# Performance work log

Hardware: AMD Instinct MI355X
Metric: run time of the kernel (lower is better)

The kernel has to match this reference:

```python
import jax, jax.numpy as jnp
import numpy as np

N_NODES = 100000
N_EDGES = 1600000
N_GRAPHS = 512
DIM = 64


def gcn_conv(x, W, b, src, dst, n):
    # PyG GCNConv: h = x @ W; add self-loops; symmetric norm D^-1/2 (A+I) D^-1/2; aggregate; + bias
    h = x @ W  # [N, H]
    loop = jnp.arange(n, dtype=src.dtype)
    s = jnp.concatenate([src, loop])
    d = jnp.concatenate([dst, loop])
    deg = jax.ops.segment_sum(jnp.ones_like(d, dtype=h.dtype), d, num_segments=n)  # in-degree incl self-loop
    dinv = jnp.where(deg > 0, jax.lax.rsqrt(deg), 0.0)
    norm = dinv[s] * dinv[d]  # [E+N]
    msg = h[s] * norm[:, None]  # gather + scale
    out = jax.ops.segment_sum(msg, d, num_segments=n)  # scatter-add
    return out + b


def global_mean_pool(x, batch, num_graphs):
    sums = jax.ops.segment_sum(x, batch, num_segments=num_graphs)
    cnts = jax.ops.segment_sum(jnp.ones((x.shape[0],), x.dtype), batch, num_segments=num_graphs)
    return sums / jnp.maximum(cnts, 1.0)[:, None]


def setup_inputs() -> dict:
    key = jax.random.key(0)
    ks = jax.random.split(key, 12)
    scale = 1.0 / np.sqrt(DIM)
    x = jax.random.normal(ks[0], (N_NODES, DIM), jnp.float32)
    edge_index = jax.random.randint(ks[1], (2, N_EDGES), 0, N_NODES, dtype=jnp.int64)
    batch = jnp.sort(jax.random.randint(ks[2], (N_NODES,), 0, N_GRAPHS, dtype=jnp.int64))
    W1 = jax.random.normal(ks[3], (DIM, DIM), jnp.float32) * scale
    b1 = jnp.zeros((DIM,), jnp.float32)
    W2 = jax.random.normal(ks[4], (DIM, DIM), jnp.float32) * scale
    b2 = jnp.zeros((DIM,), jnp.float32)
    W3 = jax.random.normal(ks[5], (DIM, DIM), jnp.float32) * scale
    b3 = jnp.zeros((DIM,), jnp.float32)
    W4 = jax.random.normal(ks[6], (DIM, 1), jnp.float32) * scale
    b4 = jnp.zeros((1,), jnp.float32)
    return {"x": x, "edge_index": edge_index, "batch": batch,
            "W1": W1, "b1": b1, "W2": W2, "b2": b2,
            "W3": W3, "b3": b3, "W4": W4, "b4": b4}


def reference(x, edge_index, batch, W1, b1, W2, b2, W3, b3, W4, b4):
    src, dst = edge_index[0], edge_index[1]
    h = gcn_conv(x, W1, b1, src, dst, N_NODES)
    h = jax.nn.relu(h)
    h = gcn_conv(h, W2, b2, src, dst, N_NODES)
    g = global_mean_pool(h, batch, N_GRAPHS)  # [G, H]
    g = jax.nn.relu(g @ W3 + b3)
    pred = (g @ W4 + b4).reshape(-1)  # [G]
    return pred
```

## Files before the change

kernel.cpp:

```cpp
#include <hip/hip_runtime.h>
#include <hip/hip_fp16.h>
#include <math.h>


#define NBLK 3125
#define BCAP 40960

__global__ __launch_bounds__(256) void k_init(float* gsum, int* blockCnt,
                                              int* bucketCursor, int gsz,
                                              int nblk) {
  int i = blockIdx.x * 256 + threadIdx.x;
  if (i < gsz) gsum[i] = 0.f;
  if (i < nblk + 64) blockCnt[i] = 0;
  if (i < 64) bucketCursor[i] = i * BCAP;
}

__global__ __launch_bounds__(256) void k_scan(const int* __restrict__ blockCnt,
                                              int* __restrict__ blockBase,
                                              int* __restrict__ blockCursor,
                                              int nblk) {
  __shared__ int wsum[4];
  int t = threadIdx.x;
  int w = t >> 6, lane = t & 63;
  int ch = (nblk + 255) >> 8;
  int lo = t * ch;
  int hi = lo + ch;
  if (hi > nblk) hi = nblk;
  int s = 0;
  for (int i = lo; i < hi; ++i) s += blockCnt[i];
  int inc = s;
  for (int off = 1; off < 64; off <<= 1) {
    int u = __shfl_up(inc, off);
    if (lane >= off) inc += u;
  }
  if (lane == 63) wsum[w] = inc;
  __syncthreads();
  int wpre = 0;
  for (int i = 0; i < w; ++i) wpre += wsum[i];
  int run = wpre + inc - s;
  for (int i = lo; i < hi; ++i) {
    int v = blockCnt[i];
    blockBase[i] = run;
    blockCursor[i] = run;
    run += v;
  }
  if (t == 0) blockBase[nblk] = wsum[0] + wsum[1] + wsum[2] + wsum[3];
}

__global__ __launch_bounds__(256) void k_p1(const int* __restrict__ src,
                                            const int* __restrict__ dst,
                                            int* __restrict__ bucketCursor,
                                            int* __restrict__ blockCnt,
                                            int* __restrict__ tmp, int e,
                                            int nblk) {
  __shared__ int hist[64];
  __shared__ int gbase[64];
  __shared__ int hB[3200];
  int t = threadIdx.x;
  for (int i = t; i < 3200; i += 256) hB[i] = 0;
  int base0 = blockIdx.x * 4096;
  for (int ph = 0; ph < 2; ++ph) {
    int base = base0 + ph * 2048;
    if (t < 64) hist[t] = 0;
    __syncthreads();
    int ent[8], rk[8], bk[8];
#pragma unroll
    for (int k = 0; k < 8; ++k) {
      int i = base + k * 256 + t;
      bool v = i < e;
      int s = v ? src[i] : 0;
      int d = v ? dst[i] : 0;
      bk[k] = d >> 11;
      ent[k] = (((d >> 5) & 63) << 22) | (s << 5) | (d & 31);
      rk[k] = v ? atomicAdd(&hist[bk[k]], 1) : -1;
      if (v) atomicAdd(&hB[d >> 5], 1);
    }
    __syncthreads();
    if (t < 64 && hist[t] > 0) gbase[t] = atomicAdd(&bucketCursor[t], hist[t]);
    __syncthreads();
#pragma unroll
    for (int k = 0; k < 8; ++k)
      if (rk[k] >= 0) {
        int pos = gbase[bk[k]] + rk[k];
        if (pos < (bk[k] + 1) * BCAP) tmp[pos] = ent[k];
      }
  }
  __syncthreads();
  for (int i = t; i < nblk; i += 256) {
    int v = hB[i];
    if (v) atomicAdd(&blockCnt[i], v);
  }
}

__global__ __launch_bounds__(256) void k_p2(const int* __restrict__ bucketCursor,
                                            const int* __restrict__ tmp,
                                            int* __restrict__ blockCursor,
                                            int* __restrict__ csr, int nblk) {
  __shared__ int hist[64];
  __shared__ int gbase[64];
  int b = blockIdx.x >> 3;
  int sl = blockIdx.x & 7;
  int lo_b = b * BCAP;
  int hi_b = bucketCursor[b];
  int len = hi_b - lo_b;
  int lo = lo_b + (int)(((long long)len * sl) >> 3);
  int hi = lo_b + (int)(((long long)len * (sl + 1)) >> 3);
  int t = threadIdx.x;
  for (int rbase = lo; rbase < hi; rbase += 2048) {
    if (t < 64) hist[t] = 0;
    __syncthreads();
    int ent[8], rk[8], bin[8];
#pragma unroll
    for (int k = 0; k < 8; ++k) {
      int i = rbase + k * 256 + t;
      bool v = i < hi;
      int en = v ? tmp[i] : 0;
      ent[k] = en;
      bin[k] = en >> 22;
      rk[k] = v ? atomicAdd(&hist[bin[k]], 1) : -1;
    }
    __syncthreads();
    if (t < 64 && hist[t] > 0)
      gbase[t] = atomicAdd(&blockCursor[(b << 6) + t], hist[t]);
    __syncthreads();
#pragma unroll
    for (int k = 0; k < 8; ++k)
      if (rk[k] >= 0) csr[gbase[bin[k]] + rk[k]] = ent[k] & 0x3FFFFF;
    __syncthreads();
  }
}

__global__ __launch_bounds__(256) void k_bsort(const int* __restrict__ blockBase,
                                               int* __restrict__ csr,
                                               float* __restrict__ dinv,
                                               int* __restrict__ segLo,
                                               int* __restrict__ segHi,
                                               const float* __restrict__ x,
                                               __half* __restrict__ P16, int n) {
  __shared__ int in_sh[1024];
  __shared__ int out_sh[1024];
  __shared__ int hist[128];
  __shared__ int hscan[128];
  __shared__ int deg[32];
  __shared__ float sdinv[32];
  int blk = blockIdx.x;
  int nodeBase = blk << 5;
  if (nodeBase >= n) return;
  int p0 = blockBase[blk];
  int p1 = blockBase[blk + 1];
  int seg = p1 - p0;
  int t = threadIdx.x;
  if (t < 32) deg[t] = 0;
  if (t == 0) {
    segLo[2 * blk] = p0;
    segHi[2 * blk] = p1;
    segLo[2 * blk + 1] = p0;
    segHi[2 * blk + 1] = p1;
  }
  __syncthreads();
  for (int i = t; i < seg; i += 256) atomicAdd(&deg[csr[p0 + i] & 31], 1);
  __syncthreads();
  if (t < 32 && nodeBase + t < n) {
    float dv = 1.0f / sqrtf((float)(deg[t] + 1));
    dinv[nodeBase + t] = dv;
    sdinv[t] = dv;
  }
  __syncthreads();
  for (int i = t; i < 1024; i += 256) {
    int row = i >> 5, h2 = (i & 31) << 1;
    int node = nodeBase + row;
    if (node < n) {
      float2 v = *(const float2*)&x[(size_t)node * 64 + h2];
      float sdv = sdinv[row];
      *(__half2*)&P16[(size_t)node * 64 + h2] =
          __floats2half2_rn(v.x * sdv, v.y * sdv);
    }
  }
  if (seg <= 0 || seg > 1024) return;
  if (t < 128) hist[t] = 0;
  __syncthreads();
  for (int i = t; i < seg; i += 256) {
    int v = csr[p0 + i];
    in_sh[i] = v;
    atomicAdd(&hist[((v & 16) << 2) | ((v >> 16) & 63)], 1);
  }
  __syncthreads();
  if (t < 64) {
    int h0 = hist[2 * t], h1 = hist[2 * t + 1];
    int s = h0 + h1;
    int inc = s;
    for (int off = 1; off < 64; off <<= 1) {
      int u = __shfl_up(inc, off);
      if (t >= off) inc += u;
    }
    hscan[2 * t] = inc - s;
    hscan[2 * t + 1] = inc - s + h0;
  }
  __syncthreads();
  int cntLow = hscan[64];
  __syncthreads();
  for (int i = t; i < seg; i += 256) {
    int v = in_sh[i];
    int pos = atomicAdd(&hscan[((v & 16) << 2) | ((v >> 16) & 63)], 1);
    out_sh[pos] = v;
  }
  __syncthreads();
  for (int i = t; i < seg; i += 256) csr[p0 + i] = out_sh[i];
  if (t == 0) {
    segHi[2 * blk] = p0 + cntLow;
    segLo[2 * blk + 1] = p0 + cntLow;
  }
}

__global__ __launch_bounds__(256) void k_gemm64brs(const float* __restrict__ X,
                                                   const float* __restrict__ W,
                                                   const float* __restrict__ bias,
                                                   const float* __restrict__ dinv,
                                                   __half* __restrict__ Y16, int n) {
  __shared__ float Xs[64 * 65];
  __shared__ float Ws[64 * 64];
  int t = threadIdx.x;
  int r0 = blockIdx.x << 6;
  for (int i = t * 4; i < 4096; i += 1024)
    *(float4*)&Ws[i] = *(const float4*)&W[i];
  for (int s = t; s < 1024; s += 256) {
    int r = s >> 4, c4 = (s & 15) << 2;
    float4 v = make_float4(0.f, 0.f, 0.f, 0.f);
    if (r0 + r < n) v = *(const float4*)&X[(size_t)(r0 + r) * 64 + c4];
    Xs[r * 65 + c4 + 0] = v.x;
    Xs[r * 65 + c4 + 1] = v.y;
    Xs[r * 65 + c4 + 2] = v.z;
    Xs[r * 65 + c4 + 3] = v.w;
  }
  __syncthreads();
  int c4 = (t & 15) << 2;
  int rb = (t >> 4) << 2;
  float4 a0 = {0, 0, 0, 0}, a1 = {0, 0, 0, 0}, a2 = {0, 0, 0, 0}, a3 = {0, 0, 0, 0};
  for (int k = 0; k < 64; ++k) {
    float4 w = *(const float4*)&Ws[k * 64 + c4];
    float x0 = Xs[(rb + 0) * 65 + k];
    float x1 = Xs[(rb + 1) * 65 + k];
    float x2 = Xs[(rb + 2) * 65 + k];
    float x3 = Xs[(rb + 3) * 65 + k];
    a0.x += x0 * w.x; a0.y += x0 * w.y; a0.z += x0 * w.z; a0.w += x0 * w.w;
    a1.x += x1 * w.x; a1.y += x1 * w.y; a1.z += x1 * w.z; a1.w += x1 * w.w;
    a2.x += x2 * w.x; a2.y += x2 * w.y; a2.z += x2 * w.z; a2.w += x2 * w.w;
    a3.x += x3 * w.x; a3.y += x3 * w.y; a3.z += x3 * w.z; a3.w += x3 * w.w;
  }
  float4 bb = *(const float4*)&bias[c4];
  int r = r0 + rb;
  union { __half2 h[2]; uint2 u; } pk;
  if (r + 0 < n) {
    float s0 = dinv[r + 0];
    pk.h[0] = __floats2half2_rn(fmaxf(a0.x + bb.x, 0.f) * s0,
                                fmaxf(a0.y + bb.y, 0.f) * s0);
    pk.h[1] = __floats2half2_rn(fmaxf(a0.z + bb.z, 0.f) * s0,
                                fmaxf(a0.w + bb.w, 0.f) * s0);
    *(uint2*)&Y16[(size_t)(r + 0) * 64 + c4] = pk.u;
  }
  if (r + 1 < n) {
    float s1 = dinv[r + 1];
    pk.h[0] = __floats2half2_rn(fmaxf(a1.x + bb.x, 0.f) * s1,
                                fmaxf(a1.y + bb.y, 0.f) * s1);
    pk.h[1] = __floats2half2_rn(fmaxf(a1.z + bb.z, 0.f) * s1,
                                fmaxf(a1.w + bb.w, 0.f) * s1);
    *(uint2*)&Y16[(size_t)(r + 1) * 64 + c4] = pk.u;
  }
  if (r + 2 < n) {
    float s2 = dinv[r + 2];
    pk.h[0] = __floats2half2_rn(fmaxf(a2.x + bb.x, 0.f) * s2,
                                fmaxf(a2.y + bb.y, 0.f) * s2);
    pk.h[1] = __floats2half2_rn(fmaxf(a2.z + bb.z, 0.f) * s2,
                                fmaxf(a2.w + bb.w, 0.f) * s2);
    *(uint2*)&Y16[(size_t)(r + 2) * 64 + c4] = pk.u;
  }
  if (r + 3 < n) {
    float s3 = dinv[r + 3];
    pk.h[0] = __floats2half2_rn(fmaxf(a3.x + bb.x, 0.f) * s3,
                                fmaxf(a3.y + bb.y, 0.f) * s3);
    pk.h[1] = __floats2half2_rn(fmaxf(a3.z + bb.z, 0.f) * s3,
                                fmaxf(a3.w + bb.w, 0.f) * s3);
    *(uint2*)&Y16[(size_t)(r + 3) * 64 + c4] = pk.u;
  }
}

template <int POOL>
__global__ __launch_bounds__(128) void k_agg(
    const __half* __restrict__ Xh, const int* __restrict__ csr,
    const int* __restrict__ segLo, const int* __restrict__ segHi,
    const float* __restrict__ dinv, const int* __restrict__ batch,
    float* __restrict__ outv, float* __restrict__ gsum, int n, int ntask) {
  __shared__ float accs[2][16 * 64];
  int t = threadIdx.x;
  int w = t >> 6, lane = t & 63;
  int task = blockIdx.x * 2 + w;
  if (task >= ntask) return;
  int nodeBase = task << 4;
  int par = task & 1;
  float* a = accs[w];
#pragma unroll 4
  for (int d = 0; d < 16; ++d) a[d * 64 + lane] = 0.f;
  int p0 = segLo[task];
  int p1 = segHi[task];
  int c = p1 - p0;
  if (c > 0) {
    int sub = lane & 31;
    int qlast = p1 - 1;
    int qq = p0 + sub;
    int pk = csr[qq < qlast ? qq : qlast];
    for (int rb = 0; rb < c; rb += 32) {
      int pk_next = 0;
      bool more = (rb + 32) < c;
      if (more) {
        int qn = p0 + rb + 32 + sub;
        pk_next = csr[qn < qlast ? qn : qlast];
      }
      int rem = c - rb;
      int ee[32];
#pragma unroll
      for (int k = 0; k < 32; ++k) ee[k] = __builtin_amdgcn_readlane(pk, k);
      __half tv[32];
#pragma unroll
      for (int k = 0; k < 32; ++k)
        tv[k] = Xh[(size_t)(ee[k] >> 5) * 64 + lane];
#pragma unroll
      for (int k = 0; k < 32; ++k)
        if (k < rem && (((ee[k] >> 4) & 1) == par))
          a[(ee[k] & 15) * 64 + lane] += __half2float(tv[k]);
      pk = pk_next;
    }
  }
  for (int d = 0; d < 16; ++d) {
    int node = nodeBase + d;
    if (node >= n) break;
    float dn = dinv[node];
    float xv = __half2float(Xh[(size_t)node * 64 + lane]);
    float v = (a[d * 64 + lane] + xv) * dn;
    if (POOL) {
      int g = batch[node];
      atomicAdd(&gsum[(size_t)g * 64 + lane], v);
    } else {
      outv[(size_t)node * 64 + lane] = v;
    }
  }
}

__global__ __launch_bounds__(256) void k_head(
    const float* __restrict__ gsum, const int* __restrict__ batch,
    const float* __restrict__ W2, const float* __restrict__ b2,
    const float* __restrict__ W3, const float* __restrict__ b3,
    const float* __restrict__ W4, const float* __restrict__ b4,
    float* __restrict__ out, int ng, int n) {
  int wid = (blockIdx.x * 256 + threadIdx.x) >> 6;
  int lane = threadIdx.x & 63;
  if (wid >= ng) return;
  int lo = 0, hi = n;
  while (lo < hi) {
    int mid = (lo + hi) >> 1;
    if (batch[mid] < wid) lo = mid + 1; else hi = mid;
  }
  int lb = lo;
  hi = n;
  while (lo < hi) {
    int mid = (lo + hi) >> 1;
    if (batch[mid] <= wid) lo = mid + 1; else hi = mid;
  }
  float cden = fmaxf((float)(lo - lb), 1.0f);
  float m = gsum[(size_t)wid * 64 + lane] / cden;
  float g2 = b2[lane];
  for (int k = 0; k < 64; ++k) {
    float mk = __shfl(m, k);
    g2 += mk * W2[k * 64 + lane];
  }
  float g3 = b3[lane];
  for (int k = 0; k < 64; ++k) {
    float gk = __shfl(g2, k);
    g3 += gk * W3[k * 64 + lane];
  }
  g3 = fmaxf(g3, 0.f);
  float r = g3 * W4[lane];
  for (int off = 32; off; off >>= 1) r += __shfl_down(r, off);
  if (lane == 0) out[wid] = r + b4[0];
}

extern "C" void kernel_launch(void* const* d_in, const int* in_sizes, int n_in,
                              void* d_out, int out_size, void* d_ws, size_t ws_size,
                              hipStream_t stream) {
  const float* x = (const float*)d_in[0];
  const int* edge = (const int*)d_in[1];
  const int* batch = (const int*)d_in[2];
  const float* W1 = (const float*)d_in[3];
  const float* b1 = (const float*)d_in[4];
  const float* W2 = (const float*)d_in[5];
  const float* b2 = (const float*)d_in[6];
  const float* W3 = (const float*)d_in[7];
  const float* b3 = (const float*)d_in[8];
  const float* W4 = (const float*)d_in[9];
  const float* b4 = (const float*)d_in[10];
  float* out = (float*)d_out;

  const int n = in_sizes[0] / 64;
  const int e = in_sizes[1] / 2;
  const int ng = out_size;
  const int* src = edge;
  const int* dst = edge + e;

  char* ws = (char*)d_ws;
  size_t off = 0;
  auto alloc = [&](size_t bytes) -> void* {
    void* p = ws + off;
    off = (off + bytes + 255) & ~(size_t)255;
    return p;
  };
  __half* A16 = (__half*)alloc((size_t)n * 64 * 2);
  float* B = (float*)alloc((size_t)n * 64 * 4);
  float* dinv = (float*)alloc((size_t)n * 4);
  int* blockCnt = (int*)alloc(3264 * 4);
  int* blockBase = (int*)alloc(3264 * 4);
  int* blockCursor = (int*)alloc(3264 * 4);
  int* bucketCursor = (int*)alloc(64 * 4);
  int* segLo = (int*)alloc(6400 * 4);
  int* segHi = (int*)alloc(6400 * 4);
  int* csr = (int*)alloc((size_t)e * 4);
  float* gsum = (float*)alloc((size_t)ng * 64 * 4);
  int* tmp = (int*)B;

  const int nblk = (n + 31) / 32;
  const int nbuck = (nblk + 63) / 64;
  const int ntask = 2 * nblk;
  const int nagg = (ntask + 1) / 2;
  const int gsz = ng * 64;

  int zmax = gsz > nblk + 64 ? gsz : nblk + 64;
  k_init<<<(zmax + 255) / 256, 256, 0, stream>>>(gsum, blockCnt, bucketCursor,
                                                 gsz, nblk);
  k_p1<<<(e + 4095) / 4096, 256, 0, stream>>>(src, dst, bucketCursor, blockCnt,
                                              tmp, e, nblk);
  k_scan<<<1, 256, 0, stream>>>(blockCnt, blockBase, blockCursor, nblk);
  k_p2<<<nbuck * 8, 256, 0, stream>>>(bucketCursor, tmp, blockCursor, csr, nblk);
  k_bsort<<<nblk, 256, 0, stream>>>(blockBase, csr, dinv, segLo, segHi, x, A16, n);

  k_agg<0><<<nagg, 128, 0, stream>>>(A16, csr, segLo, segHi, dinv, batch, B,
                                     gsum, n, ntask);
  k_gemm64brs<<<(n + 63) / 64, 256, 0, stream>>>(B, W1, b1, dinv, A16, n);
  k_agg<1><<<nagg, 128, 0, stream>>>(A16, csr, segLo, segHi, dinv, batch, B,
                                     gsum, n, ntask);
  k_head<<<((size_t)ng * 64 + 255) / 256, 256, 0, stream>>>(
      gsum, batch, W2, b2, W3, b3, W4, b4, out, ng, n);
}
```

Baseline: 297.7 us.

## Drop global scan kernel by using per-bucket padded CSR layout

Removes the single-block global prefix-scan kernel and the init kernel. Each 64-block bucket now gets a fixed BCAP-sized region in the CSR array, with a local 64-wide shuffle scan done inside k_p2, and the zeroing moves to hipMemsetAsync. k_bsort reads the segment length from blockCnt and merges its degree and histogram passes into one read of the CSR segment. This saves launches and a serial dependency, in exchange for a padded, larger CSR buffer and relative cursors.

```diff
diff --git a/kernel.cpp b/kernel.cpp
--- a/kernel.cpp
+++ b/kernel.cpp
@@ -5,47 +5,6 @@
 
 #define NBLK 3125
 #define BCAP 40960
-
-__global__ __launch_bounds__(256) void k_init(float* gsum, int* blockCnt,
-                                              int* bucketCursor, int gsz,
-                                              int nblk) {
-  int i = blockIdx.x * 256 + threadIdx.x;
-  if (i < gsz) gsum[i] = 0.f;
-  if (i < nblk + 64) blockCnt[i] = 0;
-  if (i < 64) bucketCursor[i] = i * BCAP;
-}
-
-__global__ __launch_bounds__(256) void k_scan(const int* __restrict__ blockCnt,
-                                              int* __restrict__ blockBase,
-                                              int* __restrict__ blockCursor,
-                                              int nblk) {
-  __shared__ int wsum[4];
-  int t = threadIdx.x;
-  int w = t >> 6, lane = t & 63;
-  int ch = (nblk + 255) >> 8;
-  int lo = t * ch;
-  int hi = lo + ch;
-  if (hi > nblk) hi = nblk;
-  int s = 0;
-  for (int i = lo; i < hi; ++i) s += blockCnt[i];
-  int inc = s;
-  for (int off = 1; off < 64; off <<= 1) {
-    int u = __shfl_up(inc, off);
-    if (lane >= off) inc += u;
-  }
-  if (lane == 63) wsum[w] = inc;
-  __syncthreads();
-  int wpre = 0;
-  for (int i = 0; i < w; ++i) wpre += wsum[i];
-  int run = wpre + inc - s;
-  for (int i = lo; i < hi; ++i) {
-    int v = blockCnt[i];
-    blockBase[i] = run;
-    blockCursor[i] = run;
-    run += v;
-  }
-  if (t == 0) blockBase[nblk] = wsum[0] + wsum[1] + wsum[2] + wsum[3];
-}
 
 __global__ __launch_bounds__(256) void k_p1(const int* __restrict__ src,
                                             const int* __restrict__ dst,
@@ -81,8 +40,8 @@
 #pragma unroll
     for (int k = 0; k < 8; ++k)
       if (rk[k] >= 0) {
-        int pos = gbase[bk[k]] + rk[k];
-        if (pos < (bk[k] + 1) * BCAP) tmp[pos] = ent[k];
+        int rel = gbase[bk[k]] + rk[k];
+        if (rel < BCAP) tmp[bk[k] * BCAP + rel] = ent[k];
       }
   }
   __syncthreads();
@@ -92,20 +51,37 @@
   }
 }
 
-__global__ __launch_bounds__(256) void k_p2(const int* __restrict__ bucketCursor,
+__global__ __launch_bounds__(256) void k_p2(const int* __restrict__ blockCnt,
+                                            const int* __restrict__ bucketCursor,
                                             const int* __restrict__ tmp,
                                             int* __restrict__ blockCursor,
+                                            int* __restrict__ blockBase,
                                             int* __restrict__ csr, int nblk) {
   __shared__ int hist[64];
   __shared__ int gbase[64];
+  __shared__ int base_sh[64];
   int b = blockIdx.x >> 3;
   int sl = blockIdx.x & 7;
+  int t = threadIdx.x;
+  if (t < 64) {
+    int idx = (b << 6) + t;
+    int cnt = (idx < nblk) ? blockCnt[idx] : 0;
+    int inc = cnt;
+    for (int off = 1; off < 64; off <<= 1) {
+      int u = __shfl_up(inc, off);
+      if (t >= off) inc += u;
+    }
+    int bas = b * BCAP + inc - cnt;
+    base_sh[t] = bas;
+    if (sl == 0 && idx < nblk) blockBase[idx] = bas;
+  }
+  __syncthreads();
+  int cntB = bucketCursor[b];
+  if (cntB > BCAP) cntB = BCAP;
   int lo_b = b * BCAP;
-  int hi_b = bucketCursor[b];
-  int len = hi_b - lo_b;
+  int len = cntB;
   int lo = lo_b + (int)(((long long)len * sl) >> 3);
   int hi = lo_b + (int)(((long long)len * (sl + 1)) >> 3);
-  int t = threadIdx.x;
   for (int rbase = lo; rbase < hi; rbase += 2048) {
     if (t < 64) hist[t] = 0;
     __syncthreads();
@@ -121,7 +97,7 @@
     }
     __syncthreads();
     if (t < 64 && hist[t] > 0)
-      gbase[t] = atomicAdd(&blockCursor[(b << 6) + t], hist[t]);
+      gbase[t] = base_sh[t] + atomicAdd(&blockCursor[(b << 6) + t], hist[t]);
     __syncthreads();
 #pragma unroll
     for (int k = 0; k < 8; ++k)
@@ -131,6 +107,7 @@
 }
 
 __global__ __launch_bounds__(256) void k_bsort(const int* __restrict__ blockBase,
+                                               const int* __restrict__ blockCnt,
                                                int* __restrict__ csr,
                                                float* __restrict__ dinv,
                                                int* __restrict__ segLo,
@@ -147,18 +124,29 @@
   int nodeBase = blk << 5;
   if (nodeBase >= n) return;
   int p0 = blockBase[blk];
-  int p1 = blockBase[blk + 1];
-  int seg = p1 - p0;
+  int seg = blockCnt[blk];
+  int p1e = p0 + seg;
   int t = threadIdx.x;
   if (t < 32) deg[t] = 0;
+  if (t < 128) hist[t] = 0;
   if (t == 0) {
     segLo[2 * blk] = p0;
-    segHi[2 * blk] = p1;
+    segHi[2 * blk] = p1e;
     segLo[2 * blk + 1] = p0;
-    segHi[2 * blk + 1] = p1;
-  }
-  __syncthreads();
-  for (int i = t; i < seg; i += 256) atomicAdd(&deg[csr[p0 + i] & 31], 1);
+    segHi[2 * blk + 1] = p1e;
+  }
+  __syncthreads();
+  bool sortable = (seg > 0 && seg <= 1024);
+  if (sortable) {
+    for (int i = t; i < seg; i += 256) {
+      int v = csr[p0 + i];
+      in_sh[i] = v;
+      atomicAdd(&deg[v & 31], 1);
+      atomicAdd(&hist[((v & 16) << 2) | ((v >> 16) & 63)], 1);
+    }
+  } else {
+    for (int i = t; i < seg; i += 256) atomicAdd(&deg[csr[p0 + i] & 31], 1);
+  }
   __syncthreads();
   if (t < 32 && nodeBase + t < n) {
     float dv = 1.0f / sqrtf((float)(deg[t] + 1));
@@ -176,15 +164,7 @@
           __floats2half2_rn(v.x * sdv, v.y * sdv);
     }
   }
-  if (seg <= 0 || seg > 1024) return;
-  if (t < 128) hist[t] = 0;
-  __syncthreads();
-  for (int i = t; i < seg; i += 256) {
-    int v = csr[p0 + i];
-    in_sh[i] = v;
-    atomicAdd(&hist[((v & 16) << 2) | ((v >> 16) & 63)], 1);
-  }
-  __syncthreads();
+  if (!sortable) return;
   if (t < 64) {
     int h0 = hist[2 * t], h1 = hist[2 * t + 1];
     int s = h0 + h1;
@@ -416,12 +396,12 @@
   float* B = (float*)alloc((size_t)n * 64 * 4);
   float* dinv = (float*)alloc((size_t)n * 4);
   int* blockCnt = (int*)alloc(3264 * 4);
-  int* blockBase = (int*)alloc(3264 * 4);
   int* blockCursor = (int*)alloc(3264 * 4);
   int* bucketCursor = (int*)alloc(64 * 4);
+  int* blockBase = (int*)alloc(3264 * 4);
   int* segLo = (int*)alloc(6400 * 4);
   int* segHi = (int*)alloc(6400 * 4);
-  int* csr = (int*)alloc((size_t)e * 4);
+  int* csr = (int*)alloc((size_t)64 * BCAP * 4);
   float* gsum = (float*)alloc((size_t)ng * 64 * 4);
   int* tmp = (int*)B;
 
@@ -431,14 +411,15 @@
   const int nagg = (ntask + 1) / 2;
   const int gsz = ng * 64;
 
-  int zmax = gsz > nblk + 64 ? gsz : nblk + 64;
-  k_init<<<(zmax + 255) / 256, 256, 0, stream>>>(gsum, blockCnt, bucketCursor,
-                                                 gsz, nblk);
+  size_t zspan = (size_t)((char*)(bucketCursor + 64) - (char*)blockCnt);
+  hipMemsetAsync(blockCnt, 0, zspan, stream);
+  hipMemsetAsync(gsum, 0, (size_t)gsz * 4, stream);
   k_p1<<<(e + 4095) / 4096, 256, 0, stream>>>(src, dst, bucketCursor, blockCnt,
                                               tmp, e, nblk);
-  k_scan<<<1, 256, 0, stream>>>(blockCnt, blockBase, blockCursor, nblk);
-  k_p2<<<nbuck * 8, 256, 0, stream>>>(bucketCursor, tmp, blockCursor, csr, nblk);
-  k_bsort<<<nblk, 256, 0, stream>>>(blockBase, csr, dinv, segLo, segHi, x, A16, n);
+  k_p2<<<nbuck * 8, 256, 0, stream>>>(blockCnt, bucketCursor, tmp, blockCursor,
+                                      blockBase, csr, nblk);
+  k_bsort<<<nblk, 256, 0, stream>>>(blockBase, blockCnt, csr, dinv, segLo,
+                                    segHi, x, A16, n);
 
   k_agg<0><<<nagg, 128, 0, stream>>>(A16, csr, segLo, segHi, dinv, batch, B,
                                      gsum, n, ntask);
```

New measurement: 287.4 us. 1.04x faster.
